# Performance work log

Hardware: AMD Instinct MI355X
Metric: run time of the kernel (lower is better)

Reference implementation:

```python
import jax, jax.numpy as jnp
import numpy as np

HOPS = 2

def setup_inputs() -> dict:
    key = jax.random.key(0)
    ks = jax.random.split(key, 10)
    B, n_mem, n_words, q_len, n_choices, c_len = 32, 512, 8, 32, 8, 8
    vocab, m = 50000, 256
    emb = 3 * m  # embedding_size must equal 3*mem_emb_size (u = o_q + u)
    subjects = jax.random.randint(ks[0], (B, n_mem, n_words), 0, vocab)
    relations = jax.random.randint(ks[1], (B, n_mem, n_words), 0, vocab)
    objects = jax.random.randint(ks[2], (B, n_mem, n_words), 0, vocab)
    ques = jax.random.randint(ks[3], (B, q_len), 0, vocab)
    answerChoices = jax.random.randint(ks[4], (B, n_choices, c_len), 0, vocab)
    A_tables = jax.random.normal(ks[5], (HOPS + 1, vocab, m), jnp.float32) * 0.02
    B_table = jax.random.normal(ks[6], (vocab, emb), jnp.float32) * 0.02
    U = jax.random.normal(ks[7], (emb, emb), jnp.float32) * 0.02
    V = jax.random.normal(ks[8], (emb, emb), jnp.float32) * 0.02
    W = jax.random.normal(ks[9], (emb, emb), jnp.float32) * 0.02
    return dict(subjects=subjects, relations=relations, objects=objects,
                ques=ques, answerChoices=answerChoices,
                A_tables=A_tables, B_table=B_table, U=U, V=V, W=W)


def _embed_memory(table, subjects, relations, objects):
    # gather [B, M, n_words, m], sum over words, concat s|r|o -> [B, M, 3m]
    s = table[subjects].sum(axis=2)
    r = table[relations].sum(axis=2)
    o = table[objects].sum(axis=2)
    return jnp.concatenate([s, r, o], axis=-1)


def _renorm_q(scores):
    # log_softmax shifted by row-min, then L1 renorm with 1e-8 offset (as in source)
    p = jax.nn.log_softmax(scores, axis=1)
    p = p - p.min(axis=1, keepdims=True)
    norm = jnp.abs(p + 1e-8).sum(axis=1, keepdims=True)
    return p / norm


def _renorm_a(scores):
    # log_softmax, L1 renorm with zero-norm guard (row += 1 then renorm)
    p = jax.nn.log_softmax(scores, axis=-1)
    norm = jnp.abs(p).sum(axis=-1, keepdims=True)
    p = jnp.where(norm == 0, p + 1.0, p)
    norm = jnp.abs(p).sum(axis=-1, keepdims=True)
    return p / norm


def reference(subjects, relations, objects, ques, answerChoices, A_tables, B_table, U, V, W):
    u = B_table[ques].sum(axis=1)                           # [B, emb]
    a = jnp.transpose(B_table[answerChoices].sum(axis=2), (1, 0, 2))  # [C, B, emb]
    o_q = None
    o_a = None
    for hop in range(HOPS):
        inp = _embed_memory(A_tables[hop], subjects, relations, objects)      # [B, M, 3m]
        out = _embed_memory(A_tables[hop + 1], subjects, relations, objects)  # [B, M, 3m]
        # question hop
        p_q = _renorm_q(jnp.einsum('bmd,de,be->bm', inp, U, u))
        o_q = jnp.einsum('bm,bmd->bd', p_q, out)
        u = o_q + u
        # answer-choice hops (batched over choices)
        p_a = _renorm_a(jnp.einsum('bmd,de,cbe->cbm', inp, V, a))
        o_a = jnp.einsum('cbm,bmd->cbd', p_a, out)
        a = o_a + a
    # prediction[b,c] = o_q[b] . (W @ o_a[c,b])
    return jnp.einsum('bd,de,cbe->bc', o_q, W, o_a)
```

## Files before the change

kernel.cpp:

```cpp
#include <hip/hip_runtime.h>

#define B_    32
#define M_    512
#define W_    8
#define QL    32
#define NC    8
#define CL    8
#define EMB   768
#define MDIM  256
#define VOCAB 50000
#define NV    288


__global__ __launch_bounds__(768) void init_ua(const float* __restrict__ Btab,
        const int* __restrict__ ques, const int* __restrict__ ac,
        float* __restrict__ X){
    int v = blockIdx.x, d = threadIdx.x;
    float acc = 0.f;
    if (v < 32){
        const int* q = ques + v*QL;
        for (int i=0;i<QL;i++) acc += Btab[(size_t)q[i]*EMB + d];
    } else {
        int c = (v-32)>>5, b = (v-32)&31;
        const int* q = ac + (b*NC + c)*CL;
        for (int i=0;i<CL;i++) acc += Btab[(size_t)q[i]*EMB + d];
    }
    X[(size_t)v*EMB + d] = acc;
}

__global__ __launch_bounds__(256) void proj_gemm(const float* __restrict__ X,
        const float* __restrict__ T0, const float* __restrict__ T1,
        float* __restrict__ C, int tB){
    __shared__ float Xs[32*64];
    __shared__ float Ts[64*65];
    int cb = blockIdx.x, rb = blockIdx.y;
    const float* T = (rb==0) ? T0 : T1;
    int tid = threadIdx.x;
    int col = tid & 63, rg = tid >> 6;
    int c0 = cb*64, r0 = rb*32;
    float acc[8] = {0,0,0,0,0,0,0,0};
    for (int k0=0;k0<EMB;k0+=64){
        #pragma unroll
        for (int i=0;i<8;i++){
            int eid = i*256 + tid;
            int r = eid>>6, k = eid&63;
            Xs[r*64+k] = X[(size_t)(r0+r)*EMB + k0+k];
        }
        if (tB){
            #pragma unroll
            for (int i=0;i<16;i++){
                int c = i*4 + rg;
                Ts[c*65 + col] = T[(size_t)(c0+c)*EMB + k0+col];
            }
        } else {
            #pragma unroll
            for (int i=0;i<16;i++){
                int k = i*4 + rg;
                Ts[k*65 + col] = T[(size_t)(k0+k)*EMB + c0+col];
            }
        }
        __syncthreads();
        #pragma unroll
        for (int k=0;k<64;k++){
            float tv = tB ? Ts[col*65 + k] : Ts[k*65 + col];
            #pragma unroll
            for (int i=0;i<8;i++)
                acc[i] += Xs[(rg*8+i)*64 + k] * tv;
        }
        __syncthreads();
    }
    #pragma unroll
    for (int i=0;i<8;i++)
        C[(size_t)(r0+rg*8+i)*EMB + c0+col] = acc[i];
}

__global__ __launch_bounds__(256) void scores_kernel(const float* __restrict__ A,
        const float* __restrict__ P,
        const int* __restrict__ subj, const int* __restrict__ rel,
        const int* __restrict__ obj, float* __restrict__ SC){
    int b = blockIdx.x, mc = blockIdx.y;
    int wave = threadIdx.x >> 6, lane = threadIdx.x & 63;
    int m0 = mc*16 + wave*4;
    float acc[4][9];
    #pragma unroll
    for (int i=0;i<4;i++)
        #pragma unroll
        for (int j=0;j<9;j++) acc[i][j]=0.f;
    #pragma unroll 1
    for (int slot=0; slot<3; ++slot){
        const int* base = (slot==0) ? subj : (slot==1) ? rel : obj;
        float4 pj[9];
        pj[0] = *(const float4*)(P + (size_t)b*EMB + slot*256 + lane*4);
        #pragma unroll
        for (int c=0;c<8;c++)
            pj[c+1] = *(const float4*)(P + (size_t)(32 + c*32 + b)*EMB + slot*256 + lane*4);
        const int* ids = base + (b*M_ + m0)*W_;
        #pragma unroll
        for (int mi=0;mi<4;mi++){
            #pragma unroll
            for (int w=0;w<W_;w++){
                int idx = ids[mi*W_ + w];
                float4 rv = *(const float4*)(A + (size_t)idx*MDIM + lane*4);
                #pragma unroll
                for (int j=0;j<9;j++)
                    acc[mi][j] += rv.x*pj[j].x + rv.y*pj[j].y
                                + rv.z*pj[j].z + rv.w*pj[j].w;
            }
        }
    }
    #pragma unroll
    for (int mi=0;mi<4;mi++){
        #pragma unroll
        for (int j=0;j<9;j++){
            float v = acc[mi][j];
            #pragma unroll
            for (int off=32;off;off>>=1) v += __shfl_xor(v, off, 64);
            if (lane==0){
                int vr = (j==0) ? b : 32 + (j-1)*32 + b;
                SC[(size_t)vr*M_ + m0+mi] = v;
            }
        }
    }
}

__global__ __launch_bounds__(256) void renorm_kernel(float* __restrict__ SC){
    int v = blockIdx.x, tid = threadIdx.x;
    float* row = SC + (size_t)v*M_;
    __shared__ float red[256];
    float s0 = row[tid], s1 = row[tid+256];
    float m = fmaxf(s0,s1);
    red[tid]=m; __syncthreads();
    for (int o=128;o;o>>=1){ if (tid<o) red[tid]=fmaxf(red[tid],red[tid+o]); __syncthreads(); }
    m = red[0]; __syncthreads();
    float e = expf(s0-m)+expf(s1-m);
    red[tid]=e; __syncthreads();
    for (int o=128;o;o>>=1){ if (tid<o) red[tid]+=red[tid+o]; __syncthreads(); }
    float lse = logf(red[0]); __syncthreads();
    float p0 = s0-m-lse, p1 = s1-m-lse;
    if (v < 32){
        red[tid]=fminf(p0,p1); __syncthreads();
        for (int o=128;o;o>>=1){ if (tid<o) red[tid]=fminf(red[tid],red[tid+o]); __syncthreads(); }
        float mn = red[0]; __syncthreads();
        p0 -= mn; p1 -= mn;
        red[tid]=fabsf(p0+1e-8f)+fabsf(p1+1e-8f); __syncthreads();
        for (int o=128;o;o>>=1){ if (tid<o) red[tid]+=red[tid+o]; __syncthreads(); }
        float nrm = red[0];
        p0 /= nrm; p1 /= nrm;
    } else {
        red[tid]=fabsf(p0)+fabsf(p1); __syncthreads();
        for (int o=128;o;o>>=1){ if (tid<o) red[tid]+=red[tid+o]; __syncthreads(); }
        float nrm = red[0];
        if (nrm == 0.f){ p0 += 1.f; p1 += 1.f; nrm = 512.f; }
        p0 /= nrm; p1 /= nrm;
    }
    row[tid]=p0; row[tid+256]=p1;
}

__global__ __launch_bounds__(256) void o_kernel(const float* __restrict__ A,
        const float* __restrict__ SC,
        const int* __restrict__ subj, const int* __restrict__ rel,
        const int* __restrict__ obj, float* __restrict__ Opart){
    int b = blockIdx.x, slot = blockIdx.y, chunk = blockIdx.z;
    int tid = threadIdx.x;
    __shared__ float pl[9*64];
    int m0 = chunk*64;
    for (int t=tid; t<9*64; t+=256){
        int j = t>>6, mi = t&63;
        int vr = (j==0) ? b : 32 + (j-1)*32 + b;
        pl[t] = SC[(size_t)vr*M_ + m0+mi];
    }
    __syncthreads();
    const int* ids = ((slot==0)?subj:(slot==1)?rel:obj) + (b*M_+m0)*W_;
    float acc[9] = {0,0,0,0,0,0,0,0,0};
    for (int mi=0;mi<64;mi++){
        #pragma unroll
        for (int w=0;w<W_;w++){
            int idx = ids[mi*W_+w];
            float val = A[(size_t)idx*MDIM + tid];
            #pragma unroll
            for (int j=0;j<9;j++) acc[j] += pl[j*64+mi]*val;
        }
    }
    #pragma unroll
    for (int j=0;j<9;j++){
        int vr = (j==0) ? b : 32 + (j-1)*32 + b;
        Opart[((size_t)chunk*NV + vr)*EMB + slot*256 + tid] = acc[j];
    }
}

__global__ __launch_bounds__(256) void update_kernel(const float* __restrict__ Opart,
        float* __restrict__ O, float* __restrict__ X){
    int i = blockIdx.x*256 + threadIdx.x;
    float s = 0.f;
    #pragma unroll
    for (int c=0;c<8;c++) s += Opart[(size_t)c*NV*EMB + i];
    O[i] = s;
    X[i] += s;
}

__global__ __launch_bounds__(256) void pred_kernel(const float* __restrict__ qW,
        const float* __restrict__ O, float* __restrict__ out){
    int pair = blockIdx.x*4 + (threadIdx.x>>6);
    int lane = threadIdx.x & 63;
    int c = pair >> 5, b = pair & 31;
    const float* oa = O + (size_t)(32 + c*32 + b)*EMB;
    const float* q  = qW + (size_t)b*EMB;
    float acc = 0.f;
    for (int k=lane;k<EMB;k+=64) acc += q[k]*oa[k];
    #pragma unroll
    for (int off=32;off;off>>=1) acc += __shfl_xor(acc, off, 64);
    if (lane==0) out[b*NC + c] = acc;
}

extern "C" void kernel_launch(void* const* d_in, const int* in_sizes, int n_in,
                              void* d_out, int out_size, void* d_ws, size_t ws_size,
                              hipStream_t stream){
    const int*   subj = (const int*)d_in[0];
    const int*   rel  = (const int*)d_in[1];
    const int*   obj  = (const int*)d_in[2];
    const int*   ques = (const int*)d_in[3];
    const int*   ac   = (const int*)d_in[4];
    const float* At   = (const float*)d_in[5];
    const float* Bt   = (const float*)d_in[6];
    const float* U    = (const float*)d_in[7];
    const float* V    = (const float*)d_in[8];
    const float* Wm   = (const float*)d_in[9];
    float* out = (float*)d_out;

    float* X  = (float*)d_ws;
    float* P  = X  + NV*EMB;
    float* SC = P  + NV*EMB;
    float* O  = SC + NV*M_;
    float* Op = O  + NV*EMB;
    float* qW = Op + 8*NV*EMB;

    init_ua<<<NV, 768, 0, stream>>>(Bt, ques, ac, X);
    const size_t TBL = (size_t)VOCAB*MDIM;
    for (int h=0; h<2; ++h){
        proj_gemm<<<dim3(12,9), 256, 0, stream>>>(X, U, V, P, 1);
        scores_kernel<<<dim3(32,32), 256, 0, stream>>>(At + (size_t)h*TBL, P, subj, rel, obj, SC);
        renorm_kernel<<<NV, 256, 0, stream>>>(SC);
        o_kernel<<<dim3(32,3,8), 256, 0, stream>>>(At + (size_t)(h+1)*TBL, SC, subj, rel, obj, Op);
        update_kernel<<<NV*EMB/256, 256, 0, stream>>>(Op, O, X);
    }
    proj_gemm<<<dim3(12,1), 256, 0, stream>>>(O, Wm, Wm, qW, 0);
    pred_kernel<<<64, 256, 0, stream>>>(qW, O, out);
}
```

Before: 772.5 us.

## Stage gathered embedding rows through LDS via global_load_lds in scores and output kernels

Both gather-heavy kernels now fetch each table row with 16-byte direct global-to-LDS loads, wait on them, then read the rows back from LDS for the dot products. The output kernel is also restructured so each wave handles a different memory slot with float4 per lane; the four per-wave partials are summed through shared memory at the end. The aim is wider, more efficient gathers and fewer register-held loads. In exchange it adds LDS round trips and explicit waits, and the scores loop is no longer fully unrolled across memory slots, which can reduce the number of loads in flight.

```diff
diff --git a/kernel.cpp b/kernel.cpp
--- a/kernel.cpp
+++ b/kernel.cpp
@@ -11,6 +11,12 @@
 #define VOCAB 50000
 #define NV    288
 
+
+__device__ __forceinline__ void gload_lds16(const float* g, float* l){
+    __builtin_amdgcn_global_load_lds(
+        (const __attribute__((address_space(1))) void*)g,
+        (__attribute__((address_space(3))) void*)l, 16, 0, 0);
+}
 
 __global__ __launch_bounds__(768) void init_ua(const float* __restrict__ Btab,
         const int* __restrict__ ques, const int* __restrict__ ac,
@@ -78,8 +84,10 @@
         const float* __restrict__ P,
         const int* __restrict__ subj, const int* __restrict__ rel,
         const int* __restrict__ obj, float* __restrict__ SC){
+    __shared__ __align__(16) float stage[4*8*MDIM];
     int b = blockIdx.x, mc = blockIdx.y;
     int wave = threadIdx.x >> 6, lane = threadIdx.x & 63;
+    float* ws = stage + wave*8*MDIM;
     int m0 = mc*16 + wave*4;
     float acc[4][9];
     #pragma unroll
@@ -88,19 +96,24 @@
         for (int j=0;j<9;j++) acc[i][j]=0.f;
     #pragma unroll 1
     for (int slot=0; slot<3; ++slot){
-        const int* base = (slot==0) ? subj : (slot==1) ? rel : obj;
+        const int* basei = (slot==0) ? subj : (slot==1) ? rel : obj;
         float4 pj[9];
-        pj[0] = *(const float4*)(P + (size_t)b*EMB + slot*256 + lane*4);
+        pj[0] = *(const float4*)(P + (size_t)b*EMB + slot*MDIM + lane*4);
         #pragma unroll
         for (int c=0;c<8;c++)
-            pj[c+1] = *(const float4*)(P + (size_t)(32 + c*32 + b)*EMB + slot*256 + lane*4);
-        const int* ids = base + (b*M_ + m0)*W_;
-        #pragma unroll
+            pj[c+1] = *(const float4*)(P + (size_t)(32 + c*32 + b)*EMB + slot*MDIM + lane*4);
+        const int* ids = basei + (b*M_ + m0)*W_;
+        #pragma unroll 1
         for (int mi=0;mi<4;mi++){
             #pragma unroll
             for (int w=0;w<W_;w++){
                 int idx = ids[mi*W_ + w];
-                float4 rv = *(const float4*)(A + (size_t)idx*MDIM + lane*4);
+                gload_lds16(A + (size_t)idx*MDIM + lane*4, ws + w*MDIM);
+            }
+            asm volatile("s_waitcnt vmcnt(0)" ::: "memory");
+            #pragma unroll
+            for (int w=0;w<W_;w++){
+                float4 rv = *(const float4*)(ws + w*MDIM + lane*4);
                 #pragma unroll
                 for (int j=0;j<9;j++)
                     acc[mi][j] += rv.x*pj[j].x + rv.y*pj[j].y
@@ -160,9 +173,12 @@
         const float* __restrict__ SC,
         const int* __restrict__ subj, const int* __restrict__ rel,
         const int* __restrict__ obj, float* __restrict__ Opart){
+    __shared__ __align__(16) float smem[576 + 9216];
+    float* pl    = smem;
+    float* stage = smem + 576;
+    float* red   = smem + 576;
     int b = blockIdx.x, slot = blockIdx.y, chunk = blockIdx.z;
-    int tid = threadIdx.x;
-    __shared__ float pl[9*64];
+    int tid = threadIdx.x, wave = threadIdx.x >> 6, lane = threadIdx.x & 63;
     int m0 = chunk*64;
     for (int t=tid; t<9*64; t+=256){
         int j = t>>6, mi = t&63;
@@ -171,20 +187,43 @@
     }
     __syncthreads();
     const int* ids = ((slot==0)?subj:(slot==1)?rel:obj) + (b*M_+m0)*W_;
-    float acc[9] = {0,0,0,0,0,0,0,0,0};
-    for (int mi=0;mi<64;mi++){
-        #pragma unroll
-        for (int w=0;w<W_;w++){
-            int idx = ids[mi*W_+w];
-            float val = A[(size_t)idx*MDIM + tid];
-            #pragma unroll
-            for (int j=0;j<9;j++) acc[j] += pl[j*64+mi]*val;
-        }
-    }
+    float* wsb = stage + wave*8*MDIM;
+    float4 acc[9];
+    #pragma unroll
+    for (int j=0;j<9;j++){ acc[j].x=0.f; acc[j].y=0.f; acc[j].z=0.f; acc[j].w=0.f; }
+    #pragma unroll 1
+    for (int t=0;t<16;++t){
+        int mloc = t*4 + wave;
+        #pragma unroll
+        for (int w=0;w<W_;++w){
+            int idx = ids[mloc*W_ + w];
+            gload_lds16(A + (size_t)idx*MDIM + lane*4, wsb + w*MDIM);
+        }
+        float plj[9];
+        #pragma unroll
+        for (int j=0;j<9;j++) plj[j] = pl[j*64 + mloc];
+        asm volatile("s_waitcnt vmcnt(0)" ::: "memory");
+        #pragma unroll
+        for (int w=0;w<W_;++w){
+            float4 rv = *(const float4*)(wsb + w*MDIM + lane*4);
+            #pragma unroll
+            for (int j=0;j<9;j++){
+                acc[j].x += plj[j]*rv.x; acc[j].y += plj[j]*rv.y;
+                acc[j].z += plj[j]*rv.z; acc[j].w += plj[j]*rv.w;
+            }
+        }
+    }
+    __syncthreads();
+    #pragma unroll
+    for (int j=0;j<9;j++)
+        *(float4*)(red + (size_t)(wave*9 + j)*MDIM + lane*4) = acc[j];
+    __syncthreads();
     #pragma unroll
     for (int j=0;j<9;j++){
+        float s = red[(0*9+j)*MDIM + tid] + red[(1*9+j)*MDIM + tid]
+                + red[(2*9+j)*MDIM + tid] + red[(3*9+j)*MDIM + tid];
         int vr = (j==0) ? b : 32 + (j-1)*32 + b;
-        Opart[((size_t)chunk*NV + vr)*EMB + slot*256 + tid] = acc[j];
+        Opart[((size_t)chunk*NV + vr)*EMB + slot*MDIM + tid] = s;
     }
 }
 
```

After: 838.6 us. 8.6% more time.
